# Performance work log

Hardware: AMD Instinct MI355X
Metric: run time of the kernel (lower is better)

## Reference

```python
import jax, jax.numpy as jnp
from jax import lax
import numpy as np


def _fps(xyz, M):
    # Farthest point sampling: sequential over M steps, vectorized over batch.
    B, N, _ = xyz.shape
    def body(carry, _):
        dists, far = carry                       # dists:[B,N], far:[B]
        c = xyz[jnp.arange(B), far]              # [B,3] current centroid
        d = jnp.sum((xyz - c[:, None, :]) ** 2, axis=-1)
        dists = jnp.minimum(dists, d)
        nxt = jnp.argmax(dists, axis=-1).astype(jnp.int32)
        return (dists, nxt), far
    init = (jnp.full((B, N), 1e10, xyz.dtype), jnp.zeros((B,), jnp.int32))
    _, inds = lax.scan(body, init, None, length=M)
    return inds.T                                # [B, M]


def _ball_query(xyz, new_xyz, radius, K):
    # For each centroid pick first K point indices within radius; pad with first hit.
    N = xyz.shape[1]
    d2 = jnp.sum((new_xyz[:, :, None, :] - xyz[:, None, :, :]) ** 2, axis=-1)  # [B,M,N]
    ids = jnp.where(d2 <= radius * radius, jnp.arange(N)[None, None, :], N)
    ids = jnp.sort(ids, axis=-1)[..., :K]        # [B,M,K]
    return jnp.where(ids == N, ids[..., :1], ids)


_gather = jax.vmap(lambda p, i: p[i])            # p:[N,C], i:[M,K] -> [M,K,C]


def _mlp(x, layers):
    # Shared per-point MLP (1x1 conv + ReLU chain); BN omitted as in source head.
    for w, b in layers:
        x = jax.nn.relu(jnp.einsum('bmkc,cd->bmkd', x, w) + b)
    return x


def _sa(xyz, points, M, radius, K, layers):
    # Set-abstraction: FPS -> ball query -> group (centered xyz ++ feats) -> MLP -> max over K.
    fi = _fps(xyz, M)                                        # [B,M]
    new_xyz = jnp.take_along_axis(xyz, fi[..., None], axis=1)  # [B,M,3]
    gi = _ball_query(xyz, new_xyz, radius, K)                # [B,M,K]
    g_xyz = _gather(xyz, gi) - new_xyz[:, :, None, :]        # [B,M,K,3]
    g = jnp.concatenate([g_xyz, _gather(points, gi)], axis=-1)
    return new_xyz, jnp.max(_mlp(g, layers), axis=2)         # [B,M,Cout]


def _forward(xyz, points,
             w1a, b1a, w1b, b1b, w1c, b1c,
             w2a, b2a, w2b, b2b, w2c, b2c,
             w3a, b3a, w3b, b3b, w3c, b3c,
             lin1_w, lin2_w, cls_w, cls_b):
    B = xyz.shape[0]
    x1, f1 = _sa(xyz, points, 512, 0.2, 32, [(w1a, b1a), (w1b, b1b), (w1c, b1c)])
    x2, f2 = _sa(x1, f1, 128, 0.4, 64, [(w2a, b2a), (w2b, b2b), (w2c, b2c)])
    # group_all: single group containing all 128 points, feats = [xyz ++ points] (259 ch)
    g = jnp.concatenate([x2, f2], axis=-1)[:, None]           # [B,1,128,259]
    f3 = jnp.max(_mlp(g, [(w3a, b3a), (w3b, b3b), (w3c, b3c)]), axis=2)  # [B,1,1024]
    net = f3.reshape(B, -1)
    net = jax.nn.relu(net @ lin1_w)   # linear1 (no bias) + ReLU; dropout=identity (eval)
    net = jax.nn.relu(net @ lin2_w)
    return net @ cls_w + cls_b


def setup_inputs() -> dict:
    key = jax.random.key(0)
    ks = iter(jax.random.split(key, 40))
    B, N, NC = 32, 1024, 40
    inp = {}
    inp['xyz'] = jax.random.uniform(next(ks), (B, N, 3), jnp.float32, -1.0, 1.0)
    inp['points'] = jax.random.normal(next(ks), (B, N, 3), jnp.float32)
    def lin(cin, cout):
        w = jax.random.normal(next(ks), (cin, cout), jnp.float32) / np.float32(np.sqrt(cin))
        return w, jnp.zeros((cout,), jnp.float32)
    dims = {'1': [(6, 64), (64, 64), (64, 128)],
            '2': [(131, 128), (128, 128), (128, 256)],
            '3': [(259, 256), (256, 512), (512, 1024)]}
    for s, layer_dims in dims.items():
        for tag, (ci, co) in zip('abc', layer_dims):
            w, b = lin(ci, co)
            inp['w%s%s' % (s, tag)] = w
            inp['b%s%s' % (s, tag)] = b
    inp['lin1_w'] = jax.random.normal(next(ks), (1024, 512), jnp.float32) / np.float32(32.0)
    inp['lin2_w'] = jax.random.normal(next(ks), (512, 256), jnp.float32) / np.float32(np.sqrt(512))
    inp['cls_w'] = jax.random.normal(next(ks), (256, NC), jnp.float32) / np.float32(16.0)
    inp['cls_b'] = jnp.zeros((NC,), jnp.float32)
    return inp


def reference(xyz, points,
              w1a, b1a, w1b, b1b, w1c, b1c,
              w2a, b2a, w2b, b2b, w2c, b2c,
              w3a, b3a, w3b, b3b, w3c, b3c,
              lin1_w, lin2_w, cls_w, cls_b):
    return _forward(xyz, points,
                    w1a, b1a, w1b, b1b, w1c, b1c,
                    w2a, b2a, w2b, b2b, w2c, b2c,
                    w3a, b3a, w3b, b3b, w3c, b3c,
                    lin1_w, lin2_w, cls_w, cls_b)
```

## Files before the change

kernel.cpp:

```cpp
#include <hip/hip_runtime.h>

#define DEVFN __device__ __forceinline__

static inline int ceil_div(int a, int b) { return (a + b - 1) / b; }

typedef __attribute__((ext_vector_type(8))) short         bf16x8;
typedef __attribute__((ext_vector_type(4))) float         f32x4;
typedef __attribute__((ext_vector_type(8))) unsigned short u16x8;
typedef unsigned short us;

DEVFN us f2bf(float x) {
    unsigned u = __float_as_uint(x);
    unsigned r = ((u >> 16) & 1u) + 0x7fffu;
    return (us)((u + r) >> 16);
}
DEVFN float bf2f(us h) { return __uint_as_float(((unsigned)h) << 16); }

template<int CTRL>
DEVFN double dpp_max_step(double v)
{
    int lo = __double2loint(v), hi = __double2hiint(v);
    int tlo = __builtin_amdgcn_update_dpp(lo, lo, CTRL, 0xF, 0xF, false);
    int thi = __builtin_amdgcn_update_dpp(hi, hi, CTRL, 0xF, 0xF, false);
    return fmax(v, __hiloint2double(thi, tlo));
}

template<int N>
DEVFN void fps4_body(const float* __restrict__ p, int MS,
                     int* __restrict__ oidx, float* __restrict__ onx,
                     float4* sp, double* kslots)
{
    constexpr int PPL = N / 256;
    const int tid = threadIdx.x;
    float px[PPL], py[PPL], pz[PPL], dd[PPL];
    unsigned lo[PPL];
    #pragma unroll
    for (int j = 0; j < PPL; ++j) {
        int idx = tid + 256 * j;
        px[j] = p[idx*3+0]; py[j] = p[idx*3+1]; pz[j] = p[idx*3+2];
        sp[idx] = make_float4(px[j], py[j], pz[j], 0.f);
        dd[j] = 1e10f;
        lo[j] = ~(unsigned)idx;
    }
    __syncthreads();
    int far = 0;
    for (int s = 0; s < MS; ++s) {
        float4 c4 = sp[far];
        if (tid == 0) {
            oidx[s] = far;
            onx[s*3+0] = c4.x; onx[s*3+1] = c4.y; onx[s*3+2] = c4.z;
        }
        double cand[PPL];
        #pragma unroll
        for (int j = 0; j < PPL; ++j) {
            float dx = __fsub_rn(px[j], c4.x);
            float dy = __fsub_rn(py[j], c4.y);
            float dz = __fsub_rn(pz[j], c4.z);
            float d  = __fadd_rn(__fadd_rn(__fmul_rn(dx,dx), __fmul_rn(dy,dy)),
                                 __fmul_rn(dz,dz));
            float nd = fminf(dd[j], d);
            dd[j] = nd;
            cand[j] = __hiloint2double(__float_as_int(nd), (int)lo[j]);
        }
        #pragma unroll
        for (int st = PPL/2; st > 0; st >>= 1)
            #pragma unroll
            for (int j = 0; j < PPL; ++j)
                if (j < st) cand[j] = fmax(cand[j], cand[j + st]);
        double v = cand[0];
        v = dpp_max_step<0xB1>(v);
        v = dpp_max_step<0x4E>(v);
        v = dpp_max_step<0x124>(v);
        v = dpp_max_step<0x128>(v);
        v = dpp_max_step<0x142>(v);
        v = dpp_max_step<0x143>(v);
        if ((tid & 63) == 63) kslots[(s & 1)*4 + (tid >> 6)] = v;
        __syncthreads();
        const double* ks = kslots + (s & 1)*4;
        double kx = fmax(fmax(ks[0], ks[1]), fmax(ks[2], ks[3]));
        far = (int)(~(unsigned)__double2loint(kx));
    }
}

struct WJobs {
    const float* src[8];
    us* wh[8];
    us* wl[8];
    int CItot[8], CO[8], CIpad[8], ro[8];
    int blk_off[9];
};

template<int N>
__global__ __launch_bounds__(256) void fps4_wprep_kernel(
    const float* __restrict__ xyz, int M,
    int* __restrict__ out_idx, float* __restrict__ nxout,
    int nfps, WJobs jobs)
{
    __shared__ float4 sp[N];
    __shared__ double kslots[8];
    if ((int)blockIdx.x < nfps) {
        int b = blockIdx.x;
        fps4_body<N>(xyz + (size_t)b * N * 3, M,
                     out_idx + (size_t)b * M, nxout + (size_t)b * M * 3, sp, kslots);
        return;
    }
    int wb = blockIdx.x - nfps;
    int j = 0;
    while (wb >= jobs.blk_off[j+1]) ++j;
    int t = (wb - jobs.blk_off[j]) * 256 + threadIdx.x;
    int CIpad = jobs.CIpad[j], CO = jobs.CO[j];
    if (t >= CIpad * CO) return;
    int co = t / CIpad, ci = t % CIpad;
    int src = ci + jobs.ro[j];
    float v = (src < jobs.CItot[j]) ? jobs.src[j][(size_t)src * CO + co] : 0.f;
    us h = f2bf(v);
    jobs.wh[j][t] = h;
    jobs.wl[j][t] = f2bf(v - bf2f(h));
}

__global__ void ballquery_kernel(const float* __restrict__ xyz,
                                 const float* __restrict__ new_xyz,
                                 int* __restrict__ gi,
                                 int B, int N, int M, int K, float r2)
{
    int t = blockIdx.x * blockDim.x + threadIdx.x;
    if (t >= B * M) return;
    int b = t / M;
    const float* p = xyz + (size_t)b * N * 3;
    float cx = new_xyz[t*3+0], cy = new_xyz[t*3+1], cz = new_xyz[t*3+2];
    int* out = gi + (size_t)t * K;
    int cnt = 0, first = 0;
    bool havefirst = false;
    for (int i = 0; i < N; ++i) {
        float dx = __fsub_rn(p[i*3+0], cx);
        float dy = __fsub_rn(p[i*3+1], cy);
        float dz = __fsub_rn(p[i*3+2], cz);
        float d  = __fadd_rn(__fadd_rn(__fmul_rn(dx,dx), __fmul_rn(dy,dy)),
                             __fmul_rn(dz,dz));
        if (d <= r2) {
            if (!havefirst) { first = i; havefirst = true; }
            out[cnt++] = i;
            if (cnt == K) break;
        }
    }
    for (; cnt < K; ++cnt) out[cnt] = first;
}

DEVFN float f4_elem(const float4& v, int u) {
    return u == 0 ? v.x : u == 1 ? v.y : u == 2 ? v.z : v.w;
}

__global__ __launch_bounds__(256) void sa1_l1_fps2_kernel(
    const float* __restrict__ xyz, const float* __restrict__ feats,
    const float* __restrict__ new_xyz , const int* __restrict__ gi,
    const float* __restrict__ w, const float* __restrict__ bias,
    us* __restrict__ oh, us* __restrict__ ol,
    int row0, int nb_main, int fps_on,
    int* __restrict__ fps2, float* __restrict__ nx2)
{
    __shared__ float4 sp[512];
    __shared__ double kslots[8];
    if ((int)blockIdx.x >= nb_main) {
        if (!fps_on) return;
        const int b = blockIdx.x - nb_main;
        fps4_body<512>(new_xyz + (size_t)b * 512 * 3, 128,
                       fps2 + (size_t)b * 128, nx2 + (size_t)b * 128 * 3,
                       sp, kslots);
        return;
    }
    constexpr int CF = 3, CO = 64, KPTS = 32, N = 1024, M = 512, WCH = 16;
    const int lane = threadIdx.x & 63;
    const int wv   = __builtin_amdgcn_readfirstlane(threadIdx.x >> 6);
    const int rl   = blockIdx.x * 64 + lane;
    const int row  = row0 + rl;
    const int cent = row / KPTS;
    const int b    = cent / M;
    const int idx  = gi[row];
    const float* pp  = xyz + ((size_t)b*N + idx)*3;
    const float* cc3 = new_xyz + (size_t)cent*3;
    float a0 = __fsub_rn(pp[0], cc3[0]);
    float a1 = __fsub_rn(pp[1], cc3[1]);
    float a2 = __fsub_rn(pp[2], cc3[2]);
    const float* frow = feats + ((size_t)b*N + idx)*CF;
    float f0 = frow[0], f1v = frow[1], f2v = frow[2];
    const float* wcol = w + wv*WCH;
    const float* bcol = bias + wv*WCH;
    float acc[WCH];
    #pragma unroll
    for (int j = 0; j < WCH; ++j) {
        float a = bcol[j];
        a += a0 * wcol[0*CO + j];
        a += a1 * wcol[1*CO + j];
        a += a2 * wcol[2*CO + j];
        a += f0 * wcol[3*CO + j];
        a += f1v * wcol[4*CO + j];
        a += f2v * wcol[5*CO + j];
        acc[j] = a;
    }
    #pragma unroll
    for (int j8 = 0; j8 < WCH; j8 += 8) {
        u16x8 hv, lv;
        #pragma unroll
        for (int u = 0; u < 8; ++u) {
            float v = fmaxf(acc[j8+u], 0.f);
            us h = f2bf(v);
            hv[u] = h;
            lv[u] = f2bf(v - bf2f(h));
        }
        size_t o = (size_t)rl*CO + wv*WCH + j8;
        *(u16x8*)(&oh[o]) = hv;
        *(u16x8*)(&ol[o]) = lv;
    }
}

__global__ __launch_bounds__(256) void sa1_l2_bq2_kernel(
    const us* __restrict__ ah, const us* __restrict__ al,
    const us* __restrict__ wh, const us* __restrict__ wl,
    const float* __restrict__ bias,
    us* __restrict__ oh, us* __restrict__ ol,
    int nb_main, int bq_on,
    const float* __restrict__ nx1, const float* __restrict__ nx2,
    int* __restrict__ gi2)
{
    if ((int)blockIdx.x >= nb_main) {
        if (!bq_on) return;
        int t = (blockIdx.x - nb_main) * 256 + threadIdx.x;
        if (t >= 32 * 128) return;
        constexpr int N = 512, M = 128, K = 64;
        const float r2 = (float)(0.4*0.4);
        int b = t / M;
        const float* p = nx1 + (size_t)b * N * 3;
        float cx = nx2[t*3+0], cy = nx2[t*3+1], cz = nx2[t*3+2];
        int* out = gi2 + (size_t)t * K;
        int cnt = 0, first = 0;
        bool havefirst = false;
        for (int i = 0; i < N; ++i) {
            float dx = __fsub_rn(p[i*3+0], cx);
            float dy = __fsub_rn(p[i*3+1], cy);
            float dz = __fsub_rn(p[i*3+2], cz);
            float d  = __fadd_rn(__fadd_rn(__fmul_rn(dx,dx), __fmul_rn(dy,dy)),
                                 __fmul_rn(dz,dz));
            if (d <= r2) {
                if (!havefirst) { first = i; havefirst = true; }
                out[cnt++] = i;
                if (cnt == K) break;
            }
        }
        for (; cnt < K; ++cnt) out[cnt] = first;
        return;
    }
    constexpr int CI = 64, CO = 64, KT = 2, NTILE = 4, MROW = 4;
    const int wid  = threadIdx.x >> 6;
    const int lane = threadIdx.x & 63;
    const int m    = lane & 15;
    const int kg   = lane >> 4;
    const int blockrow = blockIdx.x * (64 * MROW);
    bf16x8 Ahf[MROW * KT], Alf[MROW * KT];
    #pragma unroll
    for (int t = 0; t < MROW; ++t) {
        const us* arh = ah + (size_t)(blockrow + t*64 + wid*16 + m) * CI + kg * 8;
        const us* arl = al + (size_t)(blockrow + t*64 + wid*16 + m) * CI + kg * 8;
        #pragma unroll
        for (int kt = 0; kt < KT; ++kt) {
            Ahf[t*KT + kt] = *(const bf16x8*)(arh + kt*32);
            Alf[t*KT + kt] = *(const bf16x8*)(arl + kt*32);
        }
    }
    #pragma unroll
    for (int nt = 0; nt < NTILE; ++nt) {
        f32x4 acc[MROW];
        #pragma unroll
        for (int t = 0; t < MROW; ++t) acc[t] = (f32x4){0.f, 0.f, 0.f, 0.f};
        const us* wbh = wh + (size_t)(nt*16 + m) * CI + kg * 8;
        const us* wbl = wl + (size_t)(nt*16 + m) * CI + kg * 8;
        #pragma unroll
        for (int kt = 0; kt < KT; ++kt) {
            bf16x8 Bh = *(const bf16x8*)(wbh + kt*32);
            bf16x8 Bl = *(const bf16x8*)(wbl + kt*32);
            #pragma unroll
            for (int t = 0; t < MROW; ++t) {
                acc[t] = __builtin_amdgcn_mfma_f32_16x16x32_bf16(Ahf[t*KT+kt], Bh, acc[t], 0, 0, 0);
                acc[t] = __builtin_amdgcn_mfma_f32_16x16x32_bf16(Ahf[t*KT+kt], Bl, acc[t], 0, 0, 0);
                acc[t] = __builtin_amdgcn_mfma_f32_16x16x32_bf16(Alf[t*KT+kt], Bh, acc[t], 0, 0, 0);
            }
        }
        int dcol = nt*16 + m;
        float bv = bias[dcol];
        #pragma unroll
        for (int t = 0; t < MROW; ++t)
            #pragma unroll
            for (int r = 0; r < 4; ++r) {
                float v = fmaxf(acc[t][r] + bv, 0.f);
                size_t o = (size_t)(blockrow + t*64 + wid*16 + kg*4 + r) * CO + dcol;
                us h = f2bf(v);
                oh[o] = h;
                ol[o] = f2bf(v - bf2f(h));
            }
    }
}

template<int CI, int CO, int NTILE, int MROW, int KPTS, int OUTMODE>
__global__ __launch_bounds__(256) void mfma_layer_kernel(
    const us* __restrict__ ah, const us* __restrict__ al,
    const us* __restrict__ wh, const us* __restrict__ wl,
    const float* __restrict__ bias,
    us* __restrict__ oh, us* __restrict__ ol,
    float* __restrict__ ofp, int rowbase)
{
    constexpr int KT = CI / 32;
    static_assert(KT * MROW <= 18, "A-preload register budget");
    __shared__ float partial[4][OUTMODE >= 2 ? MROW : 1][OUTMODE >= 2 ? 16*NTILE : 1];
    const int wid  = threadIdx.x >> 6;
    const int lane = threadIdx.x & 63;
    const int m    = lane & 15;
    const int kg   = lane >> 4;
    const int blockrow = blockIdx.x * (64 * MROW);
    const int colbase  = blockIdx.y * (16 * NTILE);
    bf16x8 Ahf[MROW * KT], Alf[MROW * KT];
    #pragma unroll
    for (int t = 0; t < MROW; ++t) {
        const us* arh = ah + (size_t)(blockrow + t*64 + wid*16 + m) * CI + kg * 8;
        const us* arl = al + (size_t)(blockrow + t*64 + wid*16 + m) * CI + kg * 8;
        #pragma unroll
        for (int kt = 0; kt < KT; ++kt) {
            Ahf[t*KT + kt] = *(const bf16x8*)(arh + kt*32);
            Alf[t*KT + kt] = *(const bf16x8*)(arl + kt*32);
        }
    }
    #pragma unroll
    for (int nt = 0; nt < NTILE; ++nt) {
        f32x4 acc[MROW];
        #pragma unroll
        for (int t = 0; t < MROW; ++t) acc[t] = (f32x4){0.f, 0.f, 0.f, 0.f};
        const us* wbh = wh + (size_t)(colbase + nt*16 + m) * CI + kg * 8;
        const us* wbl = wl + (size_t)(colbase + nt*16 + m) * CI + kg * 8;
        #pragma unroll
        for (int kt = 0; kt < KT; ++kt) {
            bf16x8 Bh = *(const bf16x8*)(wbh + kt*32);
            bf16x8 Bl = *(const bf16x8*)(wbl + kt*32);
            #pragma unroll
            for (int t = 0; t < MROW; ++t) {
                acc[t] = __builtin_amdgcn_mfma_f32_16x16x32_bf16(Ahf[t*KT+kt], Bh, acc[t], 0, 0, 0);
                acc[t] = __builtin_amdgcn_mfma_f32_16x16x32_bf16(Ahf[t*KT+kt], Bl, acc[t], 0, 0, 0);
                acc[t] = __builtin_amdgcn_mfma_f32_16x16x32_bf16(Alf[t*KT+kt], Bh, acc[t], 0, 0, 0);
            }
        }
        int dcol = colbase + nt*16 + m;
        float bv = bias[dcol];
        #pragma unroll
        for (int t = 0; t < MROW; ++t) {
            float v[4];
            #pragma unroll
            for (int r = 0; r < 4; ++r) v[r] = fmaxf(acc[t][r] + bv, 0.f);
            if constexpr (OUTMODE == 0) {
                #pragma unroll
                for (int r = 0; r < 4; ++r) {
                    size_t o = (size_t)(blockrow + t*64 + wid*16 + kg*4 + r) * CO + dcol;
                    us h = f2bf(v[r]);
                    oh[o] = h;
                    ol[o] = f2bf(v[r] - bf2f(h));
                }
            } else if constexpr (OUTMODE == 1) {
                #pragma unroll
                for (int r = 0; r < 4; ++r)
                    ofp[(size_t)(blockrow + t*64 + wid*16 + kg*4 + r) * CO + dcol] = v[r];
            } else {
                float mx = fmaxf(fmaxf(v[0], v[1]), fmaxf(v[2], v[3]));
                mx = fmaxf(mx, __shfl_xor(mx, 16));
                mx = fmaxf(mx, __shfl_xor(mx, 32));
                if (lane < 16) partial[wid][t][nt*16 + m] = mx;
            }
        }
    }
    if constexpr (OUTMODE >= 2) {
        __syncthreads();
        for (int c = threadIdx.x; c < 16*NTILE; c += 256) {
            #pragma unroll
            for (int t = 0; t < MROW; ++t) {
                if constexpr (KPTS == 64) {
                    float mx = fmaxf(fmaxf(partial[0][t][c], partial[1][t][c]),
                                     fmaxf(partial[2][t][c], partial[3][t][c]));
                    int cent = (rowbase + blockrow) / 64 + t;
                    if constexpr (OUTMODE == 2) {
                        ofp[(size_t)cent*CO + colbase + c] = mx;
                    } else {
                        size_t o = (size_t)cent*CO + colbase + c;
                        us h = f2bf(mx);
                        oh[o] = h; ol[o] = f2bf(mx - bf2f(h));
                    }
                } else {
                    int cent0 = (rowbase + blockrow) / 32 + t*2;
                    float v0 = fmaxf(partial[0][t][c], partial[1][t][c]);
                    float v1 = fmaxf(partial[2][t][c], partial[3][t][c]);
                    if constexpr (OUTMODE == 2) {
                        ofp[(size_t)cent0*CO + colbase + c]     = v0;
                        ofp[(size_t)(cent0+1)*CO + colbase + c] = v1;
                    } else {
                        size_t o0 = (size_t)cent0*CO + colbase + c;
                        size_t o1 = (size_t)(cent0+1)*CO + colbase + c;
                        us h0 = f2bf(v0), h1 = f2bf(v1);
                        oh[o0] = h0; ol[o0] = f2bf(v0 - bf2f(h0));
                        oh[o1] = h1; ol[o1] = f2bf(v1 - bf2f(h1));
                    }
                }
            }
        }
    }
}

template<int NTILE, int MROW>
__global__ __launch_bounds__(256) void mfma_sa2l1_kernel(
    const float* __restrict__ sxyz, const float* __restrict__ cxyz,
    const int* __restrict__ gi,
    const us* __restrict__ f1h, const us* __restrict__ f1l,
    const float* __restrict__ w,
    const us* __restrict__ wh, const us* __restrict__ wl,
    const float* __restrict__ bias,
    us* __restrict__ oh, us* __restrict__ ol,
    int rowbase)
{
    constexpr int CI = 128, CO = 128, KT = 4, KPTS = 64, M = 128, N = 512;
    const int wid  = threadIdx.x >> 6;
    const int lane = threadIdx.x & 63;
    const int m    = lane & 15;
    const int kg   = lane >> 4;
    const int blockrow = blockIdx.x * (64 * MROW);
    const int colbase  = blockIdx.y * (16 * NTILE);
    bf16x8 Ahf[MROW * KT], Alf[MROW * KT];
    #pragma unroll
    for (int t = 0; t < MROW; ++t) {
        int grow = rowbase + blockrow + t*64 + wid*16 + m;
        int cent = grow / KPTS;
        int b    = cent / M;
        int idx  = gi[grow];
        const us* arh = f1h + ((size_t)b*N + idx) * CI + kg * 8;
        const us* arl = f1l + ((size_t)b*N + idx) * CI + kg * 8;
        #pragma unroll
        for (int kt = 0; kt < KT; ++kt) {
            Ahf[t*KT + kt] = *(const bf16x8*)(arh + kt*32);
            Alf[t*KT + kt] = *(const bf16x8*)(arl + kt*32);
        }
    }
    float dx[MROW][4], dy[MROW][4], dz[MROW][4];
    #pragma unroll
    for (int t = 0; t < MROW; ++t)
        #pragma unroll
        for (int r = 0; r < 4; ++r) {
            int grow = rowbase + blockrow + t*64 + wid*16 + kg*4 + r;
            int cent = grow / KPTS;
            int b    = cent / M;
            int idx  = gi[grow];
            const float* pp = sxyz + ((size_t)b*N + idx)*3;
            const float* cc = cxyz + (size_t)cent*3;
            dx[t][r] = __fsub_rn(pp[0], cc[0]);
            dy[t][r] = __fsub_rn(pp[1], cc[1]);
            dz[t][r] = __fsub_rn(pp[2], cc[2]);
        }
    #pragma unroll
    for (int nt = 0; nt < NTILE; ++nt) {
        f32x4 acc[MROW];
        #pragma unroll
        for (int t = 0; t < MROW; ++t) acc[t] = (f32x4){0.f, 0.f, 0.f, 0.f};
        const us* wbh = wh + (size_t)(colbase + nt*16 + m) * CI + kg * 8;
        const us* wbl = wl + (size_t)(colbase + nt*16 + m) * CI + kg * 8;
        #pragma unroll
        for (int kt = 0; kt < KT; ++kt) {
            bf16x8 Bh = *(const bf16x8*)(wbh + kt*32);
            bf16x8 Bl = *(const bf16x8*)(wbl + kt*32);
            #pragma unroll
            for (int t = 0; t < MROW; ++t) {
                acc[t] = __builtin_amdgcn_mfma_f32_16x16x32_bf16(Ahf[t*KT+kt], Bh, acc[t], 0, 0, 0);
                acc[t] = __builtin_amdgcn_mfma_f32_16x16x32_bf16(Ahf[t*KT+kt], Bl, acc[t], 0, 0, 0);
                acc[t] = __builtin_amdgcn_mfma_f32_16x16x32_bf16(Alf[t*KT+kt], Bh, acc[t], 0, 0, 0);
            }
        }
        int dcol = colbase + nt*16 + m;
        float w0 = w[0*CO + dcol], w1 = w[1*CO + dcol], w2 = w[2*CO + dcol];
        float bv = bias[dcol];
        #pragma unroll
        for (int t = 0; t < MROW; ++t)
            #pragma unroll
            for (int r = 0; r < 4; ++r) {
                float v = acc[t][r] + bv + dx[t][r]*w0 + dy[t][r]*w1 + dz[t][r]*w2;
                v = fmaxf(v, 0.f);
                size_t o = (size_t)(blockrow + t*64 + wid*16 + kg*4 + r) * CO + dcol;
                us h = f2bf(v);
                oh[o] = h;
                ol[o] = f2bf(v - bf2f(h));
            }
    }
}

__global__ void concat_split_kernel(const float* __restrict__ a, const float* __restrict__ f,
                                    us* __restrict__ oh, us* __restrict__ ol,
                                    int R, int CF, int CIpad)
{
    int t = blockIdx.x * 256 + threadIdx.x;
    if (t >= R * CIpad) return;
    int r = t / CIpad, c = t % CIpad;
    float v;
    if (c < 3) v = a[r*3 + c];
    else if (c < CF + 3) v = f[(size_t)r * CF + (c - 3)];
    else v = 0.f;
    us h = f2bf(v);
    oh[t] = h;
    ol[t] = f2bf(v - bf2f(h));
}

template<int RELU, int HASB>
__global__ __launch_bounds__(256) void fc_kernel(
    const float* __restrict__ A, const float* __restrict__ W,
    const float* __restrict__ bias, float* __restrict__ Cc,
    int Mr, int Nc, int Kd)
{
    int t = blockIdx.x * 256 + threadIdx.x;
    if (t >= Mr * Nc) return;
    int row = t / Nc, col = t % Nc;
    const float* a = A + (size_t)row * Kd;
    const float* w = W + col;
    float acc = 0.f;
    #pragma unroll 8
    for (int k = 0; k < Kd; ++k)
        acc += a[k] * w[(size_t)k * Nc];
    if (HASB) acc += bias[col];
    if (RELU) acc = fmaxf(acc, 0.f);
    Cc[t] = acc;
}

__global__ void rowmax_kernel(const float* __restrict__ in, float* __restrict__ out,
                              int B, int P, int C)
{
    int t = blockIdx.x * blockDim.x + threadIdx.x;
    if (t >= B * C) return;
    int b = t / C, c = t % C;
    const float* p = in + (size_t)b * P * C + c;
    float mx = p[0];
    for (int i = 1; i < P; ++i) mx = fmaxf(mx, p[(size_t)i * C]);
    out[t] = mx;
}

extern "C" void kernel_launch(void* const* d_in, const int* in_sizes, int n_in,
                              void* d_out, int out_size, void* d_ws, size_t ws_size,
                              hipStream_t stream)
{
    const float* xyz    = (const float*)d_in[0];
    const float* points = (const float*)d_in[1];
    const float* w1a = (const float*)d_in[2];  const float* b1a = (const float*)d_in[3];
    const float* w1b = (const float*)d_in[4];  const float* b1b = (const float*)d_in[5];
    const float* w1c = (const float*)d_in[6];  const float* b1c = (const float*)d_in[7];
    const float* w2a = (const float*)d_in[8];  const float* b2a = (const float*)d_in[9];
    const float* w2b = (const float*)d_in[10]; const float* b2b = (const float*)d_in[11];
    const float* w2c = (const float*)d_in[12]; const float* b2c = (const float*)d_in[13];
    const float* w3a = (const float*)d_in[14]; const float* b3a = (const float*)d_in[15];
    const float* w3b = (const float*)d_in[16]; const float* b3b = (const float*)d_in[17];
    const float* w3c = (const float*)d_in[18]; const float* b3c = (const float*)d_in[19];
    const float* lin1 = (const float*)d_in[20];
    const float* lin2 = (const float*)d_in[21];
    const float* clsw = (const float*)d_in[22];
    const float* clsb = (const float*)d_in[23];

    char* ws = (char*)d_ws;
    size_t off = 0;
    auto alloc = [&](size_t bytes) -> void* {
        void* p = ws + off;
        off += (bytes + 255) & ~(size_t)255;
        return p;
    };
    int*   fps1 = (int*)  alloc((size_t)32*512*4);
    float* nx1  = (float*)alloc((size_t)32*512*3*4);
    int*   gi1  = (int*)  alloc((size_t)32*512*32*4);
    int*   fps2 = (int*)  alloc((size_t)32*128*4);
    float* nx2  = (float*)alloc((size_t)32*128*3*4);
    int*   gi2  = (int*)  alloc((size_t)32*128*64*4);
    float* f2   = (float*)alloc((size_t)32*128*256*4);
    float* h3c  = (float*)alloc((size_t)4096*1024*4);
    float* f3   = (float*)alloc((size_t)32*1024*4);
    float* fc1  = (float*)alloc((size_t)32*512*4);
    float* fc2  = (float*)alloc((size_t)32*256*4);

    us* w1bh = (us*)alloc(64*64*2);     us* w1bl = (us*)alloc(64*64*2);
    us* w1ch = (us*)alloc(128*64*2);    us* w1cl = (us*)alloc(128*64*2);
    us* w2ah = (us*)alloc(128*128*2);   us* w2al = (us*)alloc(128*128*2);
    us* w2bh = (us*)alloc(128*128*2);   us* w2bl = (us*)alloc(128*128*2);
    us* w2ch = (us*)alloc(256*128*2);   us* w2cl = (us*)alloc(256*128*2);
    us* w3ah = (us*)alloc(256*288*2);   us* w3al = (us*)alloc(256*288*2);
    us* w3bh = (us*)alloc(512*256*2);   us* w3bl = (us*)alloc(512*256*2);
    us* w3ch = (us*)alloc(1024*512*2);  us* w3cl = (us*)alloc(1024*512*2);
    us* f1h  = (us*)alloc((size_t)16384*128*2);
    us* f1l  = (us*)alloc((size_t)16384*128*2);
    us* g3H  = (us*)alloc((size_t)4096*288*2);  us* g3L  = (us*)alloc((size_t)4096*288*2);
    us* h3aH = (us*)alloc((size_t)4096*256*2);  us* h3aL = (us*)alloc((size_t)4096*256*2);
    us* h3bH = (us*)alloc((size_t)4096*512*2);  us* h3bL = (us*)alloc((size_t)4096*512*2);

    size_t avail = (ws_size > off + 1024) ? (ws_size - off - 1024) : 0;
    size_t bufcap = avail / 4;
    if (bufcap > (size_t)67200000) bufcap = 67200000;
    us* Ah = (us*)alloc(bufcap); us* Al = (us*)alloc(bufcap);
    us* Bh = (us*)alloc(bufcap); us* Bl = (us*)alloc(bufcap);

    WJobs jobs;
    {
        const float* src[8] = { w1b, w1c, w2a, w2b, w2c, w3a, w3b, w3c };
        us* wh[8] = { w1bh, w1ch, w2ah, w2bh, w2ch, w3ah, w3bh, w3ch };
        us* wl[8] = { w1bl, w1cl, w2al, w2bl, w2cl, w3al, w3bl, w3cl };
        int CItot[8] = { 64, 64, 131, 128, 128, 259, 256, 512 };
        int CO[8]    = { 64, 128, 128, 128, 256, 256, 512, 1024 };
        int CIpad[8] = { 64, 64, 128, 128, 128, 288, 256, 512 };
        int ro[8]    = { 0, 0, 3, 0, 0, 0, 0, 0 };
        int cum = 0;
        for (int j = 0; j < 8; ++j) {
            jobs.src[j] = src[j]; jobs.wh[j] = wh[j]; jobs.wl[j] = wl[j];
            jobs.CItot[j] = CItot[j]; jobs.CO[j] = CO[j];
            jobs.CIpad[j] = CIpad[j]; jobs.ro[j] = ro[j];
            jobs.blk_off[j] = cum;
            cum += ceil_div(CIpad[j] * CO[j], 256);
        }
        jobs.blk_off[8] = cum;
    }

    fps4_wprep_kernel<1024><<<32 + jobs.blk_off[8], 256, 0, stream>>>(
        xyz, 512, fps1, nx1, 32, jobs);
    ballquery_kernel<<<ceil_div(32*512, 256), 256, 0, stream>>>(
        xyz, nx1, gi1, 32, 1024, 512, 32, (float)(0.2*0.2));
    {
        const int rows = 32*512*32;
        int ch = (int)((bufcap / (64*2)) & ~(size_t)1023);
        if (ch > rows) ch = rows;
        if (ch < 1024) ch = 1024;
        int first = 1;
        for (int r0 = 0; r0 < rows; r0 += ch) {
            int rc = rows - r0 < ch ? rows - r0 : ch;
            int nb1 = rc/64, nb2 = rc/256;
            sa1_l1_fps2_kernel<<<nb1 + (first ? 32 : 0), 256, 0, stream>>>(
                xyz, points, nx1, gi1, w1a, b1a, Ah, Al, r0, nb1, first, fps2, nx2);
            sa1_l2_bq2_kernel<<<nb2 + (first ? 16 : 0), 256, 0, stream>>>(
                Ah, Al, w1bh, w1bl, b1b, Bh, Bl, nb2, first, nx1, nx2, gi2);
            mfma_layer_kernel<64, 128, 8, 4, 32, 3><<<dim3(nb2, 1), 256, 0, stream>>>(
                Bh, Bl, w1ch, w1cl, b1c, f1h, f1l, nullptr, r0);
            first = 0;
        }
    }

    {
        const int rows = 32*128*64;
        int ch = (int)((bufcap / (128*2)) & ~(size_t)1023);
        if (ch > rows) ch = rows;
        if (ch < 1024) ch = 1024;
        for (int r0 = 0; r0 < rows; r0 += ch) {
            int rc = rows - r0 < ch ? rows - r0 : ch;
            mfma_sa2l1_kernel<8, 2><<<dim3(rc/128, 1), 256, 0, stream>>>(
                nx1, nx2, gi2, f1h, f1l, w2a, w2ah, w2al, b2a, Ah, Al, r0);
            mfma_layer_kernel<128, 128, 8, 4, 0, 0><<<dim3(rc/256, 1), 256, 0, stream>>>(
                Ah, Al, w2bh, w2bl, b2b, Bh, Bl, nullptr, 0);
            mfma_layer_kernel<128, 256, 16, 4, 64, 2><<<dim3(rc/256, 1), 256, 0, stream>>>(
                Bh, Bl, w2ch, w2cl, b2c, nullptr, nullptr, f2, r0);
        }
    }

    concat_split_kernel<<<ceil_div(4096*288, 256), 256, 0, stream>>>(
        nx2, f2, g3H, g3L, 4096, 256, 288);
    mfma_layer_kernel<288, 256, 2, 1, 0, 0><<<dim3(4096/64, 256/32), 256, 0, stream>>>(
        g3H, g3L, w3ah, w3al, b3a, h3aH, h3aL, nullptr, 0);
    mfma_layer_kernel<256, 512, 2, 2, 0, 0><<<dim3(4096/128, 512/32), 256, 0, stream>>>(
        h3aH, h3aL, w3bh, w3bl, b3b, h3bH, h3bL, nullptr, 0);
    mfma_layer_kernel<512, 1024, 4, 1, 0, 1><<<dim3(4096/64, 1024/64), 256, 0, stream>>>(
        h3bH, h3bL, w3ch, w3cl, b3c, nullptr, nullptr, h3c, 0);
    rowmax_kernel<<<ceil_div(32*1024, 256), 256, 0, stream>>>(h3c, f3, 32, 128, 1024);

    fc_kernel<1,0><<<ceil_div(32*512, 256), 256, 0, stream>>>(
        f3, lin1, nullptr, fc1, 32, 512, 1024);
    fc_kernel<1,0><<<ceil_div(32*256, 256), 256, 0, stream>>>(
        fc1, lin2, nullptr, fc2, 32, 256, 512);
    fc_kernel<0,1><<<ceil_div(32*40, 256), 256, 0, stream>>>(
        fc2, clsw, clsb, (float*)d_out, 32, 40, 256);
}
```

Before: 1.201 ms.

## Fuse SA2 output into SA3 input, fold global max via atomics, streamline FPS

FPS no longer stages all points in shared memory. The winning wave now publishes both its key and the centroid coordinates, so the next step reads the centroid without an LDS gather. The SA2 final layer writes its max-pooled result directly into the concatenated bf16 hi/lo SA3 input, and an extra y-block fills the xyz and padding columns, which removes the concat kernel and the f2 buffer. The SA3 last layer reduces over points with an atomicMax on the int-cast float into f3, which is zeroed by an extra y-slice of the preceding layer kernel. This drops the 16MB h3c round trip and the rowmax kernel, but relies on non-negative ReLU outputs for the integer atomicMax and adds atomic contention.

```diff
diff --git a/kernel.cpp b/kernel.cpp
--- a/kernel.cpp
+++ b/kernel.cpp
@@ -28,7 +28,7 @@
 template<int N>
 DEVFN void fps4_body(const float* __restrict__ p, int MS,
                      int* __restrict__ oidx, float* __restrict__ onx,
-                     float4* sp, double* kslots)
+                     double* kkey , float* kxyz )
 {
     constexpr int PPL = N / 256;
     const int tid = threadIdx.x;
@@ -38,24 +38,22 @@
     for (int j = 0; j < PPL; ++j) {
         int idx = tid + 256 * j;
         px[j] = p[idx*3+0]; py[j] = p[idx*3+1]; pz[j] = p[idx*3+2];
-        sp[idx] = make_float4(px[j], py[j], pz[j], 0.f);
         dd[j] = 1e10f;
         lo[j] = ~(unsigned)idx;
     }
-    __syncthreads();
     int far = 0;
+    float cx = p[0], cy = p[1], cz = p[2];
     for (int s = 0; s < MS; ++s) {
-        float4 c4 = sp[far];
         if (tid == 0) {
             oidx[s] = far;
-            onx[s*3+0] = c4.x; onx[s*3+1] = c4.y; onx[s*3+2] = c4.z;
+            onx[s*3+0] = cx; onx[s*3+1] = cy; onx[s*3+2] = cz;
         }
         double cand[PPL];
         #pragma unroll
         for (int j = 0; j < PPL; ++j) {
-            float dx = __fsub_rn(px[j], c4.x);
-            float dy = __fsub_rn(py[j], c4.y);
-            float dz = __fsub_rn(pz[j], c4.z);
+            float dx = __fsub_rn(px[j], cx);
+            float dy = __fsub_rn(py[j], cy);
+            float dz = __fsub_rn(pz[j], cz);
             float d  = __fadd_rn(__fadd_rn(__fmul_rn(dx,dx), __fmul_rn(dy,dy)),
                                  __fmul_rn(dz,dz));
             float nd = fminf(dd[j], d);
@@ -74,11 +72,29 @@
         v = dpp_max_step<0x128>(v);
         v = dpp_max_step<0x142>(v);
         v = dpp_max_step<0x143>(v);
-        if ((tid & 63) == 63) kslots[(s & 1)*4 + (tid >> 6)] = v;
+        int wlo = __builtin_amdgcn_readlane(__double2loint(v), 63);
+        int whi = __builtin_amdgcn_readlane(__double2hiint(v), 63);
+        int widx = (int)(~(unsigned)wlo);
+        if (tid == (widx & 255)) {
+            int j = widx >> 8;
+            float sx = px[0], sy = py[0], sz = pz[0];
+            #pragma unroll
+            for (int q = 1; q < PPL; ++q)
+                if (j == q) { sx = px[q]; sy = py[q]; sz = pz[q]; }
+            int base = (s & 1)*4 + (tid >> 6);
+            kkey[base] = __hiloint2double(whi, wlo);
+            kxyz[base*3+0] = sx; kxyz[base*3+1] = sy; kxyz[base*3+2] = sz;
+        }
         __syncthreads();
-        const double* ks = kslots + (s & 1)*4;
-        double kx = fmax(fmax(ks[0], ks[1]), fmax(ks[2], ks[3]));
-        far = (int)(~(unsigned)__double2loint(kx));
+        const double* kk = kkey + (s & 1)*4;
+        const float*  kc = kxyz + ((s & 1)*4)*3;
+        double k0 = kk[0], k1 = kk[1], k2 = kk[2], k3 = kk[3];
+        double kmax = fmax(fmax(k0, k1), fmax(k2, k3));
+        far = (int)(~(unsigned)__double2loint(kmax));
+        cx = kc[0]; cy = kc[1]; cz = kc[2];
+        if (k1 == kmax) { cx = kc[3]; cy = kc[4];  cz = kc[5];  }
+        if (k2 == kmax) { cx = kc[6]; cy = kc[7];  cz = kc[8];  }
+        if (k3 == kmax) { cx = kc[9]; cy = kc[10]; cz = kc[11]; }
     }
 }
 
@@ -96,12 +112,13 @@
     int* __restrict__ out_idx, float* __restrict__ nxout,
     int nfps, WJobs jobs)
 {
-    __shared__ float4 sp[N];
-    __shared__ double kslots[8];
+    __shared__ double kkey[8];
+    __shared__ float  kxyz[24];
     if ((int)blockIdx.x < nfps) {
         int b = blockIdx.x;
         fps4_body<N>(xyz + (size_t)b * N * 3, M,
-                     out_idx + (size_t)b * M, nxout + (size_t)b * M * 3, sp, kslots);
+                     out_idx + (size_t)b * M, nxout + (size_t)b * M * 3,
+                     kkey, kxyz);
         return;
     }
     int wb = blockIdx.x - nfps;
@@ -158,14 +175,14 @@
     int row0, int nb_main, int fps_on,
     int* __restrict__ fps2, float* __restrict__ nx2)
 {
-    __shared__ float4 sp[512];
-    __shared__ double kslots[8];
+    __shared__ double kkey[8];
+    __shared__ float  kxyz[24];
     if ((int)blockIdx.x >= nb_main) {
         if (!fps_on) return;
         const int b = blockIdx.x - nb_main;
         fps4_body<512>(new_xyz + (size_t)b * 512 * 3, 128,
                        fps2 + (size_t)b * 128, nx2 + (size_t)b * 128 * 3,
-                       sp, kslots);
+                       kkey, kxyz);
         return;
     }
     constexpr int CF = 3, CO = 64, KPTS = 32, N = 1024, M = 512, WCH = 16;
@@ -310,6 +327,31 @@
     constexpr int KT = CI / 32;
     static_assert(KT * MROW <= 18, "A-preload register budget");
     __shared__ float partial[4][OUTMODE >= 2 ? MROW : 1][OUTMODE >= 2 ? 16*NTILE : 1];
+
+    if constexpr (OUTMODE == 0) {
+        if (ofp != nullptr && blockIdx.y == gridDim.y - 1) {
+            int i = (blockIdx.x * 256 + threadIdx.x) * 4;
+            if (i < 32*1024) {
+                ofp[i+0] = 0.f; ofp[i+1] = 0.f; ofp[i+2] = 0.f; ofp[i+3] = 0.f;
+            }
+            return;
+        }
+    }
+    if constexpr (OUTMODE == 4) {
+        if (blockIdx.y == 1) {
+            int t = blockIdx.x * 256 + threadIdx.x;
+            if (t < 4096 * 32) {
+                int row = t >> 5, k = t & 31;
+                float v = (k < 3) ? ofp[row*3 + k] : 0.f;
+                int col = (k < 3) ? k : 259 + (k - 3);
+                size_t o = (size_t)row * 288 + col;
+                us h = f2bf(v);
+                oh[o] = h; ol[o] = f2bf(v - bf2f(h));
+            }
+            return;
+        }
+    }
+
     const int wid  = threadIdx.x >> 6;
     const int lane = threadIdx.x & 63;
     const int m    = lane & 15;
@@ -377,12 +419,22 @@
         for (int c = threadIdx.x; c < 16*NTILE; c += 256) {
             #pragma unroll
             for (int t = 0; t < MROW; ++t) {
-                if constexpr (KPTS == 64) {
+                if constexpr (OUTMODE == 5) {
+                    float mx = fmaxf(fmaxf(partial[0][t][c], partial[1][t][c]),
+                                     fmaxf(partial[2][t][c], partial[3][t][c]));
+                    int batch = (rowbase + blockrow) / 128;
+                    atomicMax((int*)&ofp[(size_t)batch*CO + colbase + c],
+                              __float_as_int(mx));
+                } else if constexpr (KPTS == 64) {
                     float mx = fmaxf(fmaxf(partial[0][t][c], partial[1][t][c]),
                                      fmaxf(partial[2][t][c], partial[3][t][c]));
                     int cent = (rowbase + blockrow) / 64 + t;
                     if constexpr (OUTMODE == 2) {
                         ofp[(size_t)cent*CO + colbase + c] = mx;
+                    } else if constexpr (OUTMODE == 4) {
+                        size_t o = (size_t)cent*288 + 3 + colbase + c;
+                        us h = f2bf(mx);
+                        oh[o] = h; ol[o] = f2bf(mx - bf2f(h));
                     } else {
                         size_t o = (size_t)cent*CO + colbase + c;
                         us h = f2bf(mx);
@@ -491,22 +543,6 @@
     }
 }
 
-__global__ void concat_split_kernel(const float* __restrict__ a, const float* __restrict__ f,
-                                    us* __restrict__ oh, us* __restrict__ ol,
-                                    int R, int CF, int CIpad)
-{
-    int t = blockIdx.x * 256 + threadIdx.x;
-    if (t >= R * CIpad) return;
-    int r = t / CIpad, c = t % CIpad;
-    float v;
-    if (c < 3) v = a[r*3 + c];
-    else if (c < CF + 3) v = f[(size_t)r * CF + (c - 3)];
-    else v = 0.f;
-    us h = f2bf(v);
-    oh[t] = h;
-    ol[t] = f2bf(v - bf2f(h));
-}
-
 template<int RELU, int HASB>
 __global__ __launch_bounds__(256) void fc_kernel(
     const float* __restrict__ A, const float* __restrict__ W,
@@ -525,18 +561,6 @@
     if (HASB) acc += bias[col];
     if (RELU) acc = fmaxf(acc, 0.f);
     Cc[t] = acc;
-}
-
-__global__ void rowmax_kernel(const float* __restrict__ in, float* __restrict__ out,
-                              int B, int P, int C)
-{
-    int t = blockIdx.x * blockDim.x + threadIdx.x;
-    if (t >= B * C) return;
-    int b = t / C, c = t % C;
-    const float* p = in + (size_t)b * P * C + c;
-    float mx = p[0];
-    for (int i = 1; i < P; ++i) mx = fmaxf(mx, p[(size_t)i * C]);
-    out[t] = mx;
 }
 
 extern "C" void kernel_launch(void* const* d_in, const int* in_sizes, int n_in,
@@ -572,8 +596,6 @@
     int*   fps2 = (int*)  alloc((size_t)32*128*4);
     float* nx2  = (float*)alloc((size_t)32*128*3*4);
     int*   gi2  = (int*)  alloc((size_t)32*128*64*4);
-    float* f2   = (float*)alloc((size_t)32*128*256*4);
-    float* h3c  = (float*)alloc((size_t)4096*1024*4);
     float* f3   = (float*)alloc((size_t)32*1024*4);
     float* fc1  = (float*)alloc((size_t)32*512*4);
     float* fc2  = (float*)alloc((size_t)32*256*4);
@@ -652,20 +674,17 @@
                 nx1, nx2, gi2, f1h, f1l, w2a, w2ah, w2al, b2a, Ah, Al, r0);
             mfma_layer_kernel<128, 128, 8, 4, 0, 0><<<dim3(rc/256, 1), 256, 0, stream>>>(
                 Ah, Al, w2bh, w2bl, b2b, Bh, Bl, nullptr, 0);
-            mfma_layer_kernel<128, 256, 16, 4, 64, 2><<<dim3(rc/256, 1), 256, 0, stream>>>(
-                Bh, Bl, w2ch, w2cl, b2c, nullptr, nullptr, f2, r0);
-        }
-    }
-
-    concat_split_kernel<<<ceil_div(4096*288, 256), 256, 0, stream>>>(
-        nx2, f2, g3H, g3L, 4096, 256, 288);
+            mfma_layer_kernel<128, 256, 16, 4, 64, 4><<<dim3(rc/256, 2), 256, 0, stream>>>(
+                Bh, Bl, w2ch, w2cl, b2c, g3H, g3L, (float*)nx2, r0);
+        }
+    }
+
     mfma_layer_kernel<288, 256, 2, 1, 0, 0><<<dim3(4096/64, 256/32), 256, 0, stream>>>(
         g3H, g3L, w3ah, w3al, b3a, h3aH, h3aL, nullptr, 0);
-    mfma_layer_kernel<256, 512, 2, 2, 0, 0><<<dim3(4096/128, 512/32), 256, 0, stream>>>(
-        h3aH, h3aL, w3bh, w3bl, b3b, h3bH, h3bL, nullptr, 0);
-    mfma_layer_kernel<512, 1024, 4, 1, 0, 1><<<dim3(4096/64, 1024/64), 256, 0, stream>>>(
-        h3bH, h3bL, w3ch, w3cl, b3c, nullptr, nullptr, h3c, 0);
-    rowmax_kernel<<<ceil_div(32*1024, 256), 256, 0, stream>>>(h3c, f3, 32, 128, 1024);
+    mfma_layer_kernel<256, 512, 2, 2, 0, 0><<<dim3(4096/128, 512/32 + 1), 256, 0, stream>>>(
+        h3aH, h3aL, w3bh, w3bl, b3b, h3bH, h3bL, f3, 0);
+    mfma_layer_kernel<512, 1024, 4, 1, 0, 5><<<dim3(4096/64, 1024/64), 256, 0, stream>>>(
+        h3bH, h3bL, w3ch, w3cl, b3c, nullptr, nullptr, f3, 0);
 
     fc_kernel<1,0><<<ceil_div(32*512, 256), 256, 0, stream>>>(
         f3, lin1, nullptr, fc1, 32, 512, 1024);
```

Measured after the change: 1.244 ms. 3.6% more time.
